# Performance work log

Measured on AMD Instinct MI355X. Metric: run time of the kernel, lower is better.

The kernel has to match this reference:

```python
import jax, jax.numpy as jnp
import numpy as np

N, E = 50000, 800000
D_IN, D_HID, D_OUT = 128, 64, 32
NEG_SLOPE = 0.2


def _gat_layer(h_in, src, dst, W, a_s, a_d, b):
    # h_in: [N, din], W: [din, dout]
    h = h_in @ W                                   # [N, dout]
    alpha_src = h @ a_s                            # [N]
    alpha_dst = h @ a_d                            # [N]
    e = jax.nn.leaky_relu(alpha_src[src] + alpha_dst[dst], NEG_SLOPE)  # [E']
    # segment softmax over incoming edges of each dst node
    m = jax.ops.segment_max(e, dst, num_segments=N)
    ex = jnp.exp(e - m[dst])
    s = jax.ops.segment_sum(ex, dst, num_segments=N)
    w = ex / s[dst]                                # [E']
    out = jax.ops.segment_sum(h[src] * w[:, None], dst, num_segments=N)
    return out + b


def setup_inputs() -> dict:
    key = jax.random.key(0)
    ks = jax.random.split(key, 16)
    x = jax.random.normal(ks[0], (N, D_IN), dtype=jnp.float32)
    edge_index = jax.random.randint(ks[1], (2, E), 0, N, dtype=jnp.int64)
    dims = [(D_IN, D_HID), (D_HID, D_HID), (D_HID, D_OUT)]
    inp = {"x": x, "edge_index": edge_index}
    for i, (din, dout) in enumerate(dims):
        sc = 1.0 / np.sqrt(din)
        inp[f"W{i}"] = jax.random.normal(ks[2 + 4 * i], (din, dout), dtype=jnp.float32) * sc
        inp[f"as{i}"] = jax.random.normal(ks[3 + 4 * i], (dout,), dtype=jnp.float32) * 0.1
        inp[f"ad{i}"] = jax.random.normal(ks[4 + 4 * i], (dout,), dtype=jnp.float32) * 0.1
        inp[f"b{i}"] = jnp.zeros((dout,), dtype=jnp.float32)
    return inp


def reference(x, edge_index, W0, as0, ad0, b0, W1, as1, ad1, b1, W2, as2, ad2, b2):
    # add self loops (PyG GATConv default)
    loop = jnp.arange(N, dtype=edge_index.dtype)
    src = jnp.concatenate([edge_index[0], loop])
    dst = jnp.concatenate([edge_index[1], loop])
    h = jax.nn.relu(_gat_layer(x, src, dst, W0, as0, ad0, b0))
    h = jax.nn.relu(_gat_layer(h, src, dst, W1, as1, ad1, b1))
    h = jnp.tanh(_gat_layer(h, src, dst, W2, as2, ad2, b2))
    return h
```

## Files before the change

### kernel.cpp

```cpp
#include <hip/hip_runtime.h>
#include <hip/hip_fp16.h>
#include <math.h>

#define N_NODES 50000
#define E_EDGES 800000
#define ETOT    (E_EDGES + N_NODES)

#define BUCK_SHIFT 9
#define BUCK_SZ   (1 << BUCK_SHIFT)
#define NBUCK ((N_NODES + BUCK_SZ - 1) >> BUCK_SHIFT)
#define BS_EPT 16
#define BS_THREADS 256
#define BS_EPB (BS_THREADS * BS_EPT)
#define BS_NBLK ((ETOT + BS_EPB - 1) / BS_EPB)

template<int DIN, int DOUT>
__global__ __launch_bounds__(256)
void gemm_alpha_kernel(const float* __restrict__ X, const float* __restrict__ W,
                       const float* __restrict__ a_s, const float* __restrict__ a_d,
                       __half* __restrict__ H16, float* __restrict__ asrc,
                       float* __restrict__ adst)
{
    constexpr int COLG = DOUT / 4;
    constexpr int ROWG = 256 / COLG;
    constexpr int BM   = ROWG * 4;
    constexpr int K4   = DIN / 4;

    __shared__ float Xl[BM * DIN];
    __shared__ float Wl[DIN * DOUT];

    const int tid = threadIdx.x;
    const int row0b = blockIdx.x * BM;

    constexpr int WV = DIN * DOUT / 4;
    for (int i = tid; i < WV; i += 256)
        ((float4*)Wl)[i] = ((const float4*)W)[i];

    constexpr int XV = BM * K4;
    for (int i = tid; i < XV; i += 256) {
        int r  = i / K4;
        int j  = i % K4;
        int gr = row0b + r;
        float4 v = make_float4(0.f, 0.f, 0.f, 0.f);
        if (gr < N_NODES) v = ((const float4*)X)[gr * K4 + j];
        *(float4*)&Xl[r * DIN + ((j ^ ((r >> 2) & 7)) << 2)] = v;
    }
    __syncthreads();

    const int tx = tid % COLG;
    const int ty = tid / COLG;
    const int r0 = ty * 4;
    const int c0 = tx * 4;
    const int swz = ty & 7;

    float acc[4][4] = {};
    for (int kk = 0; kk < DIN; kk += 4) {
        float a[4][4], w[4][4];
        const int jk = ((kk >> 2) ^ swz) << 2;
#pragma unroll
        for (int i = 0; i < 4; ++i)
            *(float4*)a[i] = *(const float4*)&Xl[(r0 + i) * DIN + jk];
#pragma unroll
        for (int j = 0; j < 4; ++j)
            *(float4*)w[j] = *(const float4*)&Wl[(kk + j) * DOUT + c0];
#pragma unroll
        for (int i = 0; i < 4; ++i)
#pragma unroll
            for (int j = 0; j < 4; ++j)
                acc[i][j] = fmaf(a[i][0], w[0][j],
                            fmaf(a[i][1], w[1][j],
                            fmaf(a[i][2], w[2][j],
                            fmaf(a[i][3], w[3][j], acc[i][j]))));
    }

    float as4[4], ad4[4];
    *(float4*)as4 = *(const float4*)&a_s[c0];
    *(float4*)ad4 = *(const float4*)&a_d[c0];

#pragma unroll
    for (int i = 0; i < 4; ++i) {
        const int gr = row0b + r0 + i;
        float ps = acc[i][0] * as4[0] + acc[i][1] * as4[1] +
                   acc[i][2] * as4[2] + acc[i][3] * as4[3];
        float pd = acc[i][0] * ad4[0] + acc[i][1] * ad4[1] +
                   acc[i][2] * ad4[2] + acc[i][3] * ad4[3];
#pragma unroll
        for (int off = COLG / 2; off >= 1; off >>= 1) {
            ps += __shfl_xor(ps, off, 64);
            pd += __shfl_xor(pd, off, 64);
        }
        if (gr < N_NODES) {
            __half2 p01 = __floats2half2_rn(acc[i][0], acc[i][1]);
            __half2 p23 = __floats2half2_rn(acc[i][2], acc[i][3]);
            uint2 pk;
            pk.x = *(unsigned int*)&p01;
            pk.y = *(unsigned int*)&p23;
            *(uint2*)&H16[gr * DOUT + c0] = pk;
            if (tx == 0) { asrc[gr] = ps; adst[gr] = pd; }
        }
    }
}

__global__ __launch_bounds__(128)
void zero98_kernel(int* __restrict__ bcnt)
{
    int i = threadIdx.x;
    if (i < NBUCK) bcnt[i] = 0;
}

__global__ __launch_bounds__(BS_THREADS)
void hist_kernel(const int* __restrict__ ei, int* __restrict__ bcnt)
{
    __shared__ int lcnt[NBUCK];
    const int t = threadIdx.x;
    for (int i = t; i < NBUCK; i += BS_THREADS) lcnt[i] = 0;
    __syncthreads();
    const int e0 = blockIdx.x * BS_EPB;
#pragma unroll
    for (int k = 0; k < BS_EPT; ++k) {
        const int eid = e0 + k * BS_THREADS + t;
        if (eid < ETOT) {
            int dst = (eid < E_EDGES) ? ei[E_EDGES + eid] : (eid - E_EDGES);
            atomicAdd(&lcnt[dst >> BUCK_SHIFT], 1);
        }
    }
    __syncthreads();
    for (int i = t; i < NBUCK; i += BS_THREADS)
        if (lcnt[i] > 0) atomicAdd(&bcnt[i], lcnt[i]);
}

__global__ __launch_bounds__(128)
void scan98_kernel(const int* __restrict__ bcnt, int* __restrict__ cur,
                   int* __restrict__ cur0)
{
    __shared__ int lds[128];
    const int t = threadIdx.x;
    const int v = (t < NBUCK) ? bcnt[t] : 0;
    lds[t] = v;
    __syncthreads();
    for (int off = 1; off < 128; off <<= 1) {
        int u = (t >= off) ? lds[t - off] : 0;
        __syncthreads();
        lds[t] += u;
        __syncthreads();
    }
    if (t < NBUCK) { cur[t] = lds[t] - v; cur0[t] = lds[t] - v; }
}

__global__ __launch_bounds__(BS_THREADS)
void binscatter_kernel(const int* __restrict__ ei, int* __restrict__ cur,
                       unsigned int* __restrict__ tmp)
{
    __shared__ int lcnt[NBUCK];
    __shared__ int lbase[NBUCK];
    const int t = threadIdx.x;
    for (int i = t; i < NBUCK; i += BS_THREADS) lcnt[i] = 0;
    __syncthreads();

    const int e0 = blockIdx.x * BS_EPB;
    unsigned int pk[BS_EPT];
    int rk[BS_EPT];
    int bk[BS_EPT];
#pragma unroll
    for (int k = 0; k < BS_EPT; ++k) {
        const int eid = e0 + k * BS_THREADS + t;
        bk[k] = -1;
        if (eid < ETOT) {
            int src, dst;
            if (eid < E_EDGES) { src = ei[eid]; dst = ei[E_EDGES + eid]; }
            else               { src = dst = eid - E_EDGES; }
            bk[k] = dst >> BUCK_SHIFT;
            pk[k] = ((unsigned int)dst << 16) | (unsigned int)src;
            rk[k] = atomicAdd(&lcnt[bk[k]], 1);
        }
    }
    __syncthreads();
    for (int i = t; i < NBUCK; i += BS_THREADS)
        if (lcnt[i] > 0) lbase[i] = atomicAdd(&cur[i], lcnt[i]);
    __syncthreads();
#pragma unroll
    for (int k = 0; k < BS_EPT; ++k)
        if (bk[k] >= 0) tmp[lbase[bk[k]] + rk[k]] = pk[k];
}

__global__ __launch_bounds__(BUCK_SZ)
void bucket_sort_kernel(const unsigned int* __restrict__ tmp,
                        const int* __restrict__ cur0,
                        const int* __restrict__ bcnt,
                        unsigned int* __restrict__ csr_pk,
                        int* __restrict__ offs)
{
    __shared__ int lcnt[BUCK_SZ];
    __shared__ int loff[BUCK_SZ];
    __shared__ int lcur[BUCK_SZ];
    const int bk = blockIdx.x;
    const int t  = threadIdx.x;
    const int base = cur0[bk];
    const int cnt  = bcnt[bk];

    lcnt[t] = 0;
    __syncthreads();
    for (int i = t; i < cnt; i += BUCK_SZ)
        atomicAdd(&lcnt[(tmp[base + i] >> 16) & (BUCK_SZ - 1)], 1);
    __syncthreads();

    const int v = lcnt[t];
    loff[t] = v;
    __syncthreads();
    for (int off = 1; off < BUCK_SZ; off <<= 1) {
        int u = (t >= off) ? loff[t - off] : 0;
        __syncthreads();
        loff[t] += u;
        __syncthreads();
    }
    const int excl = loff[t] - v;

    const int g = (bk << BUCK_SHIFT) + t;
    if (g <= N_NODES) offs[g] = base + excl;

    lcur[t] = excl;
    __syncthreads();
    for (int i = t; i < cnt; i += BUCK_SZ) {
        const unsigned int pk = tmp[base + i];
        const int l = (pk >> 16) & (BUCK_SZ - 1);
        const int pos = atomicAdd(&lcur[l], 1);
        csr_pk[base + pos] = pk;
    }
}

__global__ __launch_bounds__(256)
void edge_score_kernel(const unsigned int* __restrict__ csr_pk,
                       const float* __restrict__ asrc,
                       const float* __restrict__ adst,
                       float* __restrict__ pbuf)
{
    int i = blockIdx.x * blockDim.x + threadIdx.x;
    if (i >= ETOT) return;
    const unsigned int pk = csr_pk[i];
    float v = asrc[pk & 0xffffu] + adst[pk >> 16];
    v = (v > 0.f) ? v : 0.2f * v;
    pbuf[i] = __expf(fminf(v, 80.f));
}

template<int DOUT, int ACT>
__global__ __launch_bounds__(256)
void node_agg_kernel(const int* __restrict__ offs,
                     const unsigned int* __restrict__ csr_pk,
                     const float* __restrict__ pbuf,
                     const __half* __restrict__ H16,
                     const float* __restrict__ b,
                     float* __restrict__ out)
{
    constexpr int FL    = DOUT / 4;
    constexpr int SLOTS = 64 / FL;
    const int wv   = threadIdx.x >> 6;
    const int lane = threadIdx.x & 63;
    const int fl   = lane % FL;
    const int slot = lane / FL;
    const int node = blockIdx.x * 4 + wv;
    if (node >= N_NODES) return;

    const int beg = offs[node];
    const int end = offs[node + 1];
    const __half* __restrict__ Hf = H16 + fl * 4;

    float s = 0.f;
    float4 acc = make_float4(0.f, 0.f, 0.f, 0.f);

    for (int cb = beg; cb < end; cb += SLOTS) {
        const int eid = cb + slot;
        float p = 0.f;
        uint2 h8 = make_uint2(0u, 0u);
        if (eid < end) {
            const unsigned int pk = csr_pk[eid];
            p  = pbuf[eid];
            h8 = *(const uint2*)(Hf + (pk & 0xffffu) * DOUT);
        }
        const float2 f01 = __half22float2(*(const __half2*)&h8.x);
        const float2 f23 = __half22float2(*(const __half2*)&h8.y);
        s += p;
        acc.x = fmaf(p, f01.x, acc.x);
        acc.y = fmaf(p, f01.y, acc.y);
        acc.z = fmaf(p, f23.x, acc.z);
        acc.w = fmaf(p, f23.y, acc.w);
    }

#pragma unroll
    for (int off = FL; off < 64; off <<= 1) {
        s     += __shfl_xor(s, off, 64);
        acc.x += __shfl_xor(acc.x, off, 64);
        acc.y += __shfl_xor(acc.y, off, 64);
        acc.z += __shfl_xor(acc.z, off, 64);
        acc.w += __shfl_xor(acc.w, off, 64);
    }

    if (slot == 0) {
        const float4 bb = *(const float4*)&b[fl * 4];
        const float inv = 1.f / s;
        float4 v;
        v.x = acc.x * inv + bb.x;
        v.y = acc.y * inv + bb.y;
        v.z = acc.z * inv + bb.z;
        v.w = acc.w * inv + bb.w;
        if (ACT == 0) {
            v.x = fmaxf(v.x, 0.f); v.y = fmaxf(v.y, 0.f);
            v.z = fmaxf(v.z, 0.f); v.w = fmaxf(v.w, 0.f);
        } else {
            v.x = tanhf(v.x); v.y = tanhf(v.y);
            v.z = tanhf(v.z); v.w = tanhf(v.w);
        }
        *(float4*)&out[node * DOUT + fl * 4] = v;
    }
}


template<int DIN, int DOUT, int ACT>
static void run_layer(const float* X, const float* W, const float* a_s,
                      const float* a_d, const float* b,
                      const int* offs, const unsigned int* csr_pk,
                      float* pbuf, __half* H16, float* asrc, float* adst,
                      float* out, hipStream_t stream)
{
    constexpr int COLG = DOUT / 4;
    constexpr int BM = (256 / COLG) * 4;
    const int gemm_grid = (N_NODES + BM - 1) / BM;
    gemm_alpha_kernel<DIN, DOUT><<<gemm_grid, 256, 0, stream>>>(
        X, W, a_s, a_d, H16, asrc, adst);

    const int egrid = (ETOT + 255) / 256;
    edge_score_kernel<<<egrid, 256, 0, stream>>>(csr_pk, asrc, adst, pbuf);

    const int agg_grid = (N_NODES + 3) / 4;
    node_agg_kernel<DOUT, ACT><<<agg_grid, 256, 0, stream>>>(
        offs, csr_pk, pbuf, H16, b, out);
}

extern "C" void kernel_launch(void* const* d_in, const int* in_sizes, int n_in,
                              void* d_out, int out_size, void* d_ws, size_t ws_size,
                              hipStream_t stream)
{
    const float* x  = (const float*)d_in[0];
    const int*   ei = (const int*)d_in[1];
    const float* W0 = (const float*)d_in[2];
    const float* as0= (const float*)d_in[3];
    const float* ad0= (const float*)d_in[4];
    const float* b0 = (const float*)d_in[5];
    const float* W1 = (const float*)d_in[6];
    const float* as1= (const float*)d_in[7];
    const float* ad1= (const float*)d_in[8];
    const float* b1 = (const float*)d_in[9];
    const float* W2 = (const float*)d_in[10];
    const float* as2= (const float*)d_in[11];
    const float* ad2= (const float*)d_in[12];
    const float* b2 = (const float*)d_in[13];
    float* out = (float*)d_out;

    char* wsb = (char*)d_ws;
    auto take = [&](size_t bytes) {
        char* p = wsb;
        wsb += (bytes + 255) & ~size_t(255);
        return p;
    };
    __half* h16    = (__half*)take(sizeof(__half) * N_NODES * 64);
    float* buf_act = (float*)take(sizeof(float) * N_NODES * 64);
    float* pbuf    = (float*)take(sizeof(float) * ETOT);
    float* asrc    = (float*)take(sizeof(float) * N_NODES);
    float* adst    = (float*)take(sizeof(float) * N_NODES);
    int*   offs    = (int*)take(sizeof(int) * (N_NODES + 1));
    int*   bcnt    = (int*)take(sizeof(int) * NBUCK);
    int*   cur     = (int*)take(sizeof(int) * NBUCK);
    int*   cur0    = (int*)take(sizeof(int) * NBUCK);
    unsigned int* csr_pk = (unsigned int*)take(sizeof(unsigned int) * ETOT);
    unsigned int* tmp = (unsigned int*)h16;

    const int egrid = (ETOT + 255) / 256;
    zero98_kernel<<<1, 128, 0, stream>>>(bcnt);
    hist_kernel<<<BS_NBLK, BS_THREADS, 0, stream>>>(ei, bcnt);
    scan98_kernel<<<1, 128, 0, stream>>>(bcnt, cur, cur0);
    binscatter_kernel<<<BS_NBLK, BS_THREADS, 0, stream>>>(ei, cur, tmp);
    bucket_sort_kernel<<<NBUCK, BUCK_SZ, 0, stream>>>(tmp, cur0, bcnt,
                                                      csr_pk, offs);

    run_layer<128, 64, 0>(x, W0, as0, ad0, b0, offs, csr_pk, pbuf,
                          h16, asrc, adst, buf_act, stream);
    run_layer<64, 64, 0>(buf_act, W1, as1, ad1, b1, offs, csr_pk, pbuf,
                         h16, asrc, adst, buf_act, stream);
    run_layer<64, 32, 1>(buf_act, W2, as2, ad2, b2, offs, csr_pk, pbuf,
                         h16, asrc, adst, out, stream);
}
```

Measured before the change: 203.9 us.

## Fuse edge score computation into node aggregation and widen per-lane feature loads

Removes the separate edge_score kernel and its pbuf round trip. Each aggregation lane now recomputes the leaky-relu/exp score from asrc and the node's adst. Each lane also loads 8 half features (uint4) instead of 4, so more edges are handled per wave iteration. The next csr entry is prefetched one iteration ahead. This saves a launch and an E-sized write/read, at the cost of redundant exp work across feature lanes and more registers per lane.

```diff
diff --git a/kernel.cpp b/kernel.cpp
--- a/kernel.cpp
+++ b/kernel.cpp
@@ -228,30 +228,17 @@
     }
 }
 
-__global__ __launch_bounds__(256)
-void edge_score_kernel(const unsigned int* __restrict__ csr_pk,
-                       const float* __restrict__ asrc,
-                       const float* __restrict__ adst,
-                       float* __restrict__ pbuf)
-{
-    int i = blockIdx.x * blockDim.x + threadIdx.x;
-    if (i >= ETOT) return;
-    const unsigned int pk = csr_pk[i];
-    float v = asrc[pk & 0xffffu] + adst[pk >> 16];
-    v = (v > 0.f) ? v : 0.2f * v;
-    pbuf[i] = __expf(fminf(v, 80.f));
-}
-
 template<int DOUT, int ACT>
 __global__ __launch_bounds__(256)
 void node_agg_kernel(const int* __restrict__ offs,
                      const unsigned int* __restrict__ csr_pk,
-                     const float* __restrict__ pbuf,
+                     const float* __restrict__ asrc,
+                     const float* __restrict__ adst,
                      const __half* __restrict__ H16,
                      const float* __restrict__ b,
                      float* __restrict__ out)
 {
-    constexpr int FL    = DOUT / 4;
+    constexpr int FL    = DOUT / 8;
     constexpr int SLOTS = 64 / FL;
     const int wv   = threadIdx.x >> 6;
     const int lane = threadIdx.x & 63;
@@ -262,54 +249,65 @@
 
     const int beg = offs[node];
     const int end = offs[node + 1];
-    const __half* __restrict__ Hf = H16 + fl * 4;
+    const float adn = adst[node];
+    const __half* __restrict__ Hf = H16 + fl * 8;
 
     float s = 0.f;
-    float4 acc = make_float4(0.f, 0.f, 0.f, 0.f);
+    float acc[8] = {};
+
+    int eid = beg + slot;
+    bool valid = (eid < end);
+    unsigned int pk = valid ? csr_pk[eid] : 0u;
 
     for (int cb = beg; cb < end; cb += SLOTS) {
-        const int eid = cb + slot;
+        const int nid = cb + SLOTS + slot;
+        const bool nvalid = (nid < end);
+        const unsigned int npk = nvalid ? csr_pk[nid] : 0u;
+
         float p = 0.f;
-        uint2 h8 = make_uint2(0u, 0u);
-        if (eid < end) {
-            const unsigned int pk = csr_pk[eid];
-            p  = pbuf[eid];
-            h8 = *(const uint2*)(Hf + (pk & 0xffffu) * DOUT);
-        }
-        const float2 f01 = __half22float2(*(const __half2*)&h8.x);
-        const float2 f23 = __half22float2(*(const __half2*)&h8.y);
+        uint4 h = make_uint4(0u, 0u, 0u, 0u);
+        if (valid) {
+            const unsigned int src = pk & 0xffffu;
+            float v = asrc[src] + adn;
+            v = fmaxf(v, 0.2f * v);
+            p = __expf(fminf(v, 80.f));
+            h = *(const uint4*)(Hf + src * DOUT);
+        }
+        const float2 f0 = __half22float2(*(const __half2*)&h.x);
+        const float2 f1 = __half22float2(*(const __half2*)&h.y);
+        const float2 f2 = __half22float2(*(const __half2*)&h.z);
+        const float2 f3 = __half22float2(*(const __half2*)&h.w);
         s += p;
-        acc.x = fmaf(p, f01.x, acc.x);
-        acc.y = fmaf(p, f01.y, acc.y);
-        acc.z = fmaf(p, f23.x, acc.z);
-        acc.w = fmaf(p, f23.y, acc.w);
+        acc[0] = fmaf(p, f0.x, acc[0]);
+        acc[1] = fmaf(p, f0.y, acc[1]);
+        acc[2] = fmaf(p, f1.x, acc[2]);
+        acc[3] = fmaf(p, f1.y, acc[3]);
+        acc[4] = fmaf(p, f2.x, acc[4]);
+        acc[5] = fmaf(p, f2.y, acc[5]);
+        acc[6] = fmaf(p, f3.x, acc[6]);
+        acc[7] = fmaf(p, f3.y, acc[7]);
+        valid = nvalid;
+        pk = npk;
     }
 
 #pragma unroll
     for (int off = FL; off < 64; off <<= 1) {
-        s     += __shfl_xor(s, off, 64);
-        acc.x += __shfl_xor(acc.x, off, 64);
-        acc.y += __shfl_xor(acc.y, off, 64);
-        acc.z += __shfl_xor(acc.z, off, 64);
-        acc.w += __shfl_xor(acc.w, off, 64);
+        s += __shfl_xor(s, off, 64);
+#pragma unroll
+        for (int j = 0; j < 8; ++j)
+            acc[j] += __shfl_xor(acc[j], off, 64);
     }
 
     if (slot == 0) {
-        const float4 bb = *(const float4*)&b[fl * 4];
         const float inv = 1.f / s;
-        float4 v;
-        v.x = acc.x * inv + bb.x;
-        v.y = acc.y * inv + bb.y;
-        v.z = acc.z * inv + bb.z;
-        v.w = acc.w * inv + bb.w;
-        if (ACT == 0) {
-            v.x = fmaxf(v.x, 0.f); v.y = fmaxf(v.y, 0.f);
-            v.z = fmaxf(v.z, 0.f); v.w = fmaxf(v.w, 0.f);
-        } else {
-            v.x = tanhf(v.x); v.y = tanhf(v.y);
-            v.z = tanhf(v.z); v.w = tanhf(v.w);
-        }
-        *(float4*)&out[node * DOUT + fl * 4] = v;
+        float o[8];
+#pragma unroll
+        for (int j = 0; j < 8; ++j) {
+            float v = acc[j] * inv + b[fl * 8 + j];
+            o[j] = (ACT == 0) ? fmaxf(v, 0.f) : tanhf(v);
+        }
+        *(float4*)&out[node * DOUT + fl * 8]     = *(float4*)&o[0];
+        *(float4*)&out[node * DOUT + fl * 8 + 4] = *(float4*)&o[4];
     }
 }
 
@@ -318,7 +316,7 @@
 static void run_layer(const float* X, const float* W, const float* a_s,
                       const float* a_d, const float* b,
                       const int* offs, const unsigned int* csr_pk,
-                      float* pbuf, __half* H16, float* asrc, float* adst,
+                      __half* H16, float* asrc, float* adst,
                       float* out, hipStream_t stream)
 {
     constexpr int COLG = DOUT / 4;
@@ -327,12 +325,9 @@
     gemm_alpha_kernel<DIN, DOUT><<<gemm_grid, 256, 0, stream>>>(
         X, W, a_s, a_d, H16, asrc, adst);
 
-    const int egrid = (ETOT + 255) / 256;
-    edge_score_kernel<<<egrid, 256, 0, stream>>>(csr_pk, asrc, adst, pbuf);
-
     const int agg_grid = (N_NODES + 3) / 4;
     node_agg_kernel<DOUT, ACT><<<agg_grid, 256, 0, stream>>>(
-        offs, csr_pk, pbuf, H16, b, out);
+        offs, csr_pk, asrc, adst, H16, b, out);
 }
 
 extern "C" void kernel_launch(void* const* d_in, const int* in_sizes, int n_in,
@@ -363,7 +358,6 @@
     };
     __half* h16    = (__half*)take(sizeof(__half) * N_NODES * 64);
     float* buf_act = (float*)take(sizeof(float) * N_NODES * 64);
-    float* pbuf    = (float*)take(sizeof(float) * ETOT);
     float* asrc    = (float*)take(sizeof(float) * N_NODES);
     float* adst    = (float*)take(sizeof(float) * N_NODES);
     int*   offs    = (int*)take(sizeof(int) * (N_NODES + 1));
@@ -373,7 +367,6 @@
     unsigned int* csr_pk = (unsigned int*)take(sizeof(unsigned int) * ETOT);
     unsigned int* tmp = (unsigned int*)h16;
 
-    const int egrid = (ETOT + 255) / 256;
     zero98_kernel<<<1, 128, 0, stream>>>(bcnt);
     hist_kernel<<<BS_NBLK, BS_THREADS, 0, stream>>>(ei, bcnt);
     scan98_kernel<<<1, 128, 0, stream>>>(bcnt, cur, cur0);
@@ -381,10 +374,10 @@
     bucket_sort_kernel<<<NBUCK, BUCK_SZ, 0, stream>>>(tmp, cur0, bcnt,
                                                       csr_pk, offs);
 
-    run_layer<128, 64, 0>(x, W0, as0, ad0, b0, offs, csr_pk, pbuf,
+    run_layer<128, 64, 0>(x, W0, as0, ad0, b0, offs, csr_pk,
                           h16, asrc, adst, buf_act, stream);
-    run_layer<64, 64, 0>(buf_act, W1, as1, ad1, b1, offs, csr_pk, pbuf,
+    run_layer<64, 64, 0>(buf_act, W1, as1, ad1, b1, offs, csr_pk,
                          h16, asrc, adst, buf_act, stream);
-    run_layer<64, 32, 1>(buf_act, W2, as2, ad2, b2, offs, csr_pk, pbuf,
+    run_layer<64, 32, 1>(buf_act, W2, as2, ad2, b2, offs, csr_pk,
                          h16, asrc, adst, out, stream);
 }
```

Result: faster. 184.6 us (-9.5%).
